# Performance work log

Measured on AMD Instinct MI355X. Metric: run time of the kernel, lower is better.

## Reference

```python
import jax, jax.numpy as jnp
import numpy as np

THR = 1.0   # snntorch default threshold
BETA = 0.9  # beta_val from init_kwargs (clamped to [0,1] in snntorch)
ALPHA_SG = 2.0  # snntorch ATan surrogate default alpha

T, B, IN, H1, H2, OUT = 50, 256, 1536, 4096, 4096, 64


@jax.custom_vjp
def spike_fn(mem_shift):
    # Heaviside spike with ATan surrogate gradient (snntorch default)
    return (mem_shift > 0).astype(mem_shift.dtype)

def _spike_fwd(m):
    return spike_fn(m), m

def _spike_bwd(m, g):
    grad = (ALPHA_SG / 2.0) / (1.0 + (jnp.pi / 2.0 * ALPHA_SG * m) ** 2)
    return (g * grad,)

spike_fn.defvjp(_spike_fwd, _spike_bwd)


def setup_inputs() -> dict:
    key = jax.random.key(0)
    ks = jax.random.split(key, 7)
    spike_seq = (jax.random.uniform(ks[0], (T, B, IN)) < 0.3).astype(jnp.float32)
    def lin(k, fan_out, fan_in):
        bound = 1.0 / np.sqrt(fan_in)
        kw, kb = jax.random.split(k)
        W = jax.random.uniform(kw, (fan_out, fan_in), minval=-bound, maxval=bound, dtype=jnp.float32)
        b = jax.random.uniform(kb, (fan_out,), minval=-bound, maxval=bound, dtype=jnp.float32)
        return W, b
    W1, b1 = lin(ks[1], H1, IN)
    W2, b2 = lin(ks[2], H2, H1)
    W3, b3 = lin(ks[3], OUT, H2)
    return {"spike_seq": spike_seq, "W1": W1, "b1": b1, "W2": W2, "b2": b2, "W3": W3, "b3": b3}


def _lif_step(mem, cur):
    # snntorch Leaky, reset_mechanism='subtract': reset is computed from the
    # PREVIOUS membrane and detached; then mem = beta*mem + cur - reset*thr.
    reset = jax.lax.stop_gradient((mem > THR).astype(cur.dtype))
    mem = BETA * mem + cur - reset * THR
    spk = spike_fn(mem - THR)
    return spk, mem


def reference(spike_seq, W1, b1, W2, b2, W3, b3):
    batch = spike_seq.shape[1]
    dt = spike_seq.dtype
    m1 = jnp.zeros((batch, W1.shape[0]), dt)
    m2 = jnp.zeros((batch, W2.shape[0]), dt)
    m3 = jnp.zeros((batch, W3.shape[0]), dt)
    acc = jnp.zeros((batch, W3.shape[0]), dt)

    def step(carry, x_t):
        m1, m2, m3, acc = carry
        s1, m1 = _lif_step(m1, x_t @ W1.T + b1)
        s2, m2 = _lif_step(m2, s1 @ W2.T + b2)
        s3, m3 = _lif_step(m3, s2 @ W3.T + b3)
        return (m1, m2, m3, acc + s3), None

    (m1, m2, m3, acc), _ = jax.lax.scan(step, (m1, m2, m3, acc), spike_seq)
    return acc
```

## Files before the change

kernel.cpp:

```cpp
#include <hip/hip_runtime.h>
#include <stdint.h>
#include <stddef.h>
#include <math.h>


#define T_STEPS 50
#define BATCH   256
#define N_H     4096
#define DEN     8355711

typedef unsigned short u16;
typedef __attribute__((ext_vector_type(4))) int i32x4;
typedef __attribute__((ext_vector_type(4))) float f32x4;

#define GLL16(gp, lp) __builtin_amdgcn_global_load_lds( \
    (const __attribute__((address_space(1))) void*)(gp), \
    (__attribute__((address_space(3))) void*)(lp), 16, 0, 0)

__global__ __launch_bounds__(256) void zero_ws(float4* __restrict__ p) {
    p[(size_t)blockIdx.x * 256 + threadIdx.x] = make_float4(0.f, 0.f, 0.f, 0.f);
}

__device__ inline void digits3(float w, float inv_s, int& h, int& m, int& l) {
    int V = (int)rintf(w * inv_s);
    V = min(max(V, -DEN), DEN);
    l = ((V + 128) & 255) - 128;
    const int V2 = (V - l) >> 8;
    m = ((V2 + 128) & 255) - 128;
    h = (V2 - m) >> 8;
}

__global__ __launch_bounds__(256)
void split3_i8(const float4* __restrict__ W, char* __restrict__ P,
               size_t plane_elems, float inv_s)
{
    const size_t i = (size_t)blockIdx.x * 256 + threadIdx.x;
    const float4 w = W[i];
    int h0,m0,l0,h1,m1,l1,h2,m2,l2,h3,m3,l3;
    digits3(w.x, inv_s, h0, m0, l0);
    digits3(w.y, inv_s, h1, m1, l1);
    digits3(w.z, inv_s, h2, m2, l2);
    digits3(w.w, inv_s, h3, m3, l3);
    const uint32_t ph = (uint32_t)(uint8_t)h0 | ((uint32_t)(uint8_t)h1 << 8) |
                        ((uint32_t)(uint8_t)h2 << 16) | ((uint32_t)(uint8_t)h3 << 24);
    const uint32_t pm = (uint32_t)(uint8_t)m0 | ((uint32_t)(uint8_t)m1 << 8) |
                        ((uint32_t)(uint8_t)m2 << 16) | ((uint32_t)(uint8_t)m3 << 24);
    const uint32_t pl = (uint32_t)(uint8_t)l0 | ((uint32_t)(uint8_t)l1 << 8) |
                        ((uint32_t)(uint8_t)l2 << 16) | ((uint32_t)(uint8_t)l3 << 24);
    *(uint32_t*)&P[4 * i]                   = ph;
    *(uint32_t*)&P[plane_elems + 4 * i]     = pm;
    *(uint32_t*)&P[2 * plane_elems + 4 * i] = pl;
}

__global__ __launch_bounds__(256)
void xcvt_i8(const float4* __restrict__ in, uint32_t* __restrict__ out) {
    const size_t i = (size_t)blockIdx.x * 256 + threadIdx.x;
    const float4 v = in[i];
    out[i] = (uint32_t)(v.x > 0.5f) | ((uint32_t)(v.y > 0.5f) << 8) |
             ((uint32_t)(v.z > 0.5f) << 16) | ((uint32_t)(v.w > 0.5f) << 24);
}

template<int K>
__global__ __launch_bounds__(256, 2)
void gemm_planes(const char* __restrict__ A, const char* __restrict__ Wp,
                 float* __restrict__ cur, float s_base)
{
    const int ITERS = 3 * K / 64;
    __shared__ char As[2 * 8192];
    __shared__ char Bs[2 * 8192];

    const int tid  = threadIdx.x;
    const int wave = tid >> 6, lane = tid & 63;
    const int wm = wave >> 1, wn = wave & 1;

    const int bid   = blockIdx.x;
    const int cbase = (((bid & 7) << 2) + ((bid >> 3) & 3)) * 128;
    const int abase = (bid >> 5) * 128;

    i32x4 acc[4][4];
    f32x4 facc[4][4];
#pragma unroll
    for (int i = 0; i < 4; ++i)
#pragma unroll
        for (int j = 0; j < 4; ++j) { acc[i][j] = (i32x4)(0); facc[i][j] = (f32x4)(0.f); }

    const int soff0 = wave * 2048 + lane * 16;
    const int soff1 = soff0 + 1024;
    const int r0 = soff0 >> 6, r1 = soff1 >> 6;
    const int kb0 = ((((soff0 >> 4) & 3) ^ ((r0 >> 1) & 3)) << 4);
    const int kb1 = ((((soff1 >> 4) & 3) ^ ((r1 >> 1) & 3)) << 4);

    const size_t aoff0 = (size_t)(abase + r0) * K + kb0;
    const size_t aoff1 = (size_t)(abase + r1) * K + kb1;
    const size_t boff0 = (size_t)(cbase + r0) * K + kb0;
    const size_t boff1 = (size_t)(cbase + r1) * K + kb1;

    const int sbase = wave * 2048;

    const int rlo = lane & 15, rhi = lane >> 4;
    const int qr = (rlo >> 1) & 3;
    const int rdA = (wm * 64 + rlo) * 64 + ((rhi ^ qr) << 4);
    const int rdB = (wn * 64 + rlo) * 64 + ((rhi ^ qr) << 4);

    {
        const char* ak = A;
        const char* bk = Wp;
        GLL16(ak + aoff0, As + sbase);
        GLL16(ak + aoff1, As + sbase + 1024);
        GLL16(bk + boff0, Bs + sbase);
        GLL16(bk + boff1, Bs + sbase + 1024);
    }
    __syncthreads();

    for (int it = 0; it < ITERS; ++it) {
        const int buf = (it & 1) * 8192;
        if (it + 1 < ITERS) {
            const int fn = (it + 1) * 64;
            const int pn = fn / K;
            const int kn = fn - pn * K;
            const int nbuf = 8192 - buf;
            const char* ak = A + kn;
            const char* bk = Wp + (size_t)pn * ((size_t)N_H * K) + kn;
            GLL16(ak + aoff0, As + nbuf + sbase);
            GLL16(ak + aoff1, As + nbuf + sbase + 1024);
            GLL16(bk + boff0, Bs + nbuf + sbase);
            GLL16(bk + boff1, Bs + nbuf + sbase + 1024);
        }

        const char* pAf = As + buf + rdA;
        const char* pBf = Bs + buf + rdB;
        i32x4 av[4], bv[4];
#pragma unroll
        for (int i = 0; i < 4; ++i) av[i] = *(const i32x4*)(pAf + i * 1024);
#pragma unroll
        for (int j = 0; j < 4; ++j) bv[j] = *(const i32x4*)(pBf + j * 1024);
#pragma unroll
        for (int i = 0; i < 4; ++i)
#pragma unroll
            for (int j = 0; j < 4; ++j)
                acc[i][j] = __builtin_amdgcn_mfma_i32_16x16x64_i8(
                    av[i], bv[j], acc[i][j], 0, 0, 0);

        if ((((it + 1) * 64) % K) == 0) {
            const int p = (it * 64) / K;
            const float sc = s_base * (float)(65536 >> (8 * p));
#pragma unroll
            for (int i = 0; i < 4; ++i)
#pragma unroll
                for (int j = 0; j < 4; ++j) {
#pragma unroll
                    for (int r = 0; r < 4; ++r)
                        facc[i][j][r] += sc * (float)acc[i][j][r];
                    acc[i][j] = (i32x4)(0);
                }
        }
        __syncthreads();
    }

    const int orow = abase + wm * 64 + rhi * 4;
    const int ocol = cbase + wn * 64 + rlo;
#pragma unroll
    for (int i = 0; i < 4; ++i)
#pragma unroll
        for (int j = 0; j < 4; ++j)
#pragma unroll
            for (int r = 0; r < 4; ++r)
                cur[(size_t)(orow + i * 16 + r) * N_H + ocol + j * 16] = facc[i][j][r];
}

__global__ __launch_bounds__(256, 2)
void gemm3_i8(const char* __restrict__ A, const char* __restrict__ W3p,
              float* __restrict__ part3, float s_base)
{
    __shared__ char As[2 * 8192];
    __shared__ char Bs[2 * 4096];

    const int tid  = threadIdx.x;
    const int wave = tid >> 6, lane = tid & 63;
    const int wm = wave >> 1, wn = wave & 1;

    const int rowbase = blockIdx.x * 128;
    const int z = blockIdx.y;
    const int p = z >> 1;
    const int kstart = (z & 1) * 2048;

    i32x4 acc[4][2];
#pragma unroll
    for (int i = 0; i < 4; ++i)
#pragma unroll
        for (int j = 0; j < 2; ++j) acc[i][j] = (i32x4)(0);

    const int soff0 = wave * 2048 + lane * 16;
    const int soff1 = soff0 + 1024;
    const int r0 = soff0 >> 6, r1 = soff1 >> 6;
    const int kb0 = ((((soff0 >> 4) & 3) ^ ((r0 >> 1) & 3)) << 4);
    const int kb1 = ((((soff1 >> 4) & 3) ^ ((r1 >> 1) & 3)) << 4);
    const int soffB = tid * 16;
    const int rB = soffB >> 6;
    const int kbB = ((((soffB >> 4) & 3) ^ ((rB >> 1) & 3)) << 4);

    const size_t aoff0 = (size_t)(rowbase + r0) * 4096 + kb0;
    const size_t aoff1 = (size_t)(rowbase + r1) * 4096 + kb1;
    const size_t boff  = (size_t)rB * 4096 + kbB;

    const char* Bp = W3p + (size_t)p * 64 * 4096;
    const int sbase = wave * 2048;
    const int sbaseB = wave * 1024;

    const int rlo = lane & 15, rhi = lane >> 4;
    const int qr = (rlo >> 1) & 3;
    const int rdA = (wm * 64 + rlo) * 64 + ((rhi ^ qr) << 4);
    const int rdB = (wn * 32 + rlo) * 64 + ((rhi ^ qr) << 4);

    {
        GLL16(A + kstart + aoff0, As + sbase);
        GLL16(A + kstart + aoff1, As + sbase + 1024);
        GLL16(Bp + kstart + boff, Bs + sbaseB);
    }
    __syncthreads();

    for (int it = 0; it < 32; ++it) {
        const int bufA = (it & 1) * 8192;
        const int bufB = (it & 1) * 4096;
        if (it + 1 < 32) {
            const int kn = kstart + (it + 1) * 64;
            GLL16(A + kn + aoff0, As + (8192 - bufA) + sbase);
            GLL16(A + kn + aoff1, As + (8192 - bufA) + sbase + 1024);
            GLL16(Bp + kn + boff, Bs + (4096 - bufB) + sbaseB);
        }

        const char* pAf = As + bufA + rdA;
        const char* pBf = Bs + bufB + rdB;
        i32x4 av[4], bv[2];
#pragma unroll
        for (int i = 0; i < 4; ++i) av[i] = *(const i32x4*)(pAf + i * 1024);
#pragma unroll
        for (int j = 0; j < 2; ++j) bv[j] = *(const i32x4*)(pBf + j * 1024);
#pragma unroll
        for (int i = 0; i < 4; ++i)
#pragma unroll
            for (int j = 0; j < 2; ++j)
                acc[i][j] = __builtin_amdgcn_mfma_i32_16x16x64_i8(
                    av[i], bv[j], acc[i][j], 0, 0, 0);
        __syncthreads();
    }

    const float sc = s_base * (float)(65536 >> (8 * p));
    float* pout = part3 + (size_t)z * (12800 * 64);
    const int orow = rowbase + wm * 64 + rhi * 4;
    const int ocol = wn * 32 + rlo;
#pragma unroll
    for (int i = 0; i < 4; ++i)
#pragma unroll
        for (int j = 0; j < 2; ++j)
#pragma unroll
            for (int r = 0; r < 4; ++r)
                pout[(size_t)(orow + i * 16 + r) * 64 + ocol + j * 16] =
                    (float)acc[i][j][r] * sc;
}

__global__ __launch_bounds__(256)
void lif_scan(const float* __restrict__ cur, const float* __restrict__ bias,
              float* __restrict__ mem, char* __restrict__ sout)
{
    const int i4  = blockIdx.x * 256 + threadIdx.x;
    const int col = (i4 << 2) & (N_H - 1);
    const int b   = i4 >> 10;
    const float4 bv = *(const float4*)&bias[col];
    const size_t mbase = (size_t)b * N_H + col;
    float4 m = *(const float4*)&mem[mbase];

    for (int t = 0; t < 25; ++t) {
        const size_t off = ((size_t)t * BATCH + b) * N_H + col;
        const float4 cv = *(const float4*)&cur[off];
        float4 mn;
        { const float c = cv.x + bv.x;
          mn.x = 0.9f * m.x + c - ((m.x > 1.0f) ? 1.0f : 0.0f); }
        { const float c = cv.y + bv.y;
          mn.y = 0.9f * m.y + c - ((m.y > 1.0f) ? 1.0f : 0.0f); }
        { const float c = cv.z + bv.z;
          mn.z = 0.9f * m.z + c - ((m.z > 1.0f) ? 1.0f : 0.0f); }
        { const float c = cv.w + bv.w;
          mn.w = 0.9f * m.w + c - ((m.w > 1.0f) ? 1.0f : 0.0f); }
        const uint32_t sp = (uint32_t)(mn.x > 1.0f) | ((uint32_t)(mn.y > 1.0f) << 8) |
                            ((uint32_t)(mn.z > 1.0f) << 16) | ((uint32_t)(mn.w > 1.0f) << 24);
        *(uint32_t*)&sout[off] = sp;
        m = mn;
    }
    *(float4*)&mem[mbase] = m;
}

template<int NG>
__global__ __launch_bounds__(256)
void lif3_scan(const float* __restrict__ part, const float* __restrict__ b3,
               float* __restrict__ out)
{
    const int g = blockIdx.x * 256 + threadIdx.x;
    const int j = g & 63;
    const int b = g >> 6;
    const float bj = b3[j];
    float m = 0.f, accum = 0.f;
    for (int t = 0; t < T_STEPS; ++t) {
        const size_t row = (size_t)t * 256 + b;
        float cur = bj;
#pragma unroll
        for (int q = 0; q < NG; ++q)
            cur += part[(size_t)q * (12800 * 64) + row * 64 + j];
        const float reset = (m > 1.0f) ? 1.0f : 0.0f;
        m = 0.9f * m + cur - reset;
        accum += (m > 1.0f) ? 1.0f : 0.0f;
    }
    out[g] = accum;
}

template<int K, bool PACK_BITS>
__global__ __launch_bounds__(512)
void gemm_lif(const float* __restrict__ A, const float* __restrict__ W,
              const float* __restrict__ bias, float* __restrict__ mem,
              float* __restrict__ s_f32, uint32_t* __restrict__ s_bits)
{
    __shared__ float Asf[32][68];
    __shared__ float Wsf[32][68];
    __shared__ uint8_t us[64][64];

    const int tid = threadIdx.x;
    const int abase = blockIdx.y * 64;
    const int cbase = blockIdx.x * 64;
    const int tx = tid & 15;
    const int ty = tid >> 4;

    float acc[2][4];
#pragma unroll
    for (int i = 0; i < 2; ++i)
#pragma unroll
        for (int j = 0; j < 4; ++j) acc[i][j] = 0.f;

    const int lrow = tid >> 3;
    const int lg = tid & 7;

    for (int k0 = 0; k0 < K; k0 += 32) {
        const float4 av = *(const float4*)&A[(size_t)(abase + lrow) * K + k0 + lg * 4];
        const float4 wv = *(const float4*)&W[(size_t)(cbase + lrow) * K + k0 + lg * 4];
        __syncthreads();
        Asf[lg * 4 + 0][lrow] = av.x; Asf[lg * 4 + 1][lrow] = av.y;
        Asf[lg * 4 + 2][lrow] = av.z; Asf[lg * 4 + 3][lrow] = av.w;
        Wsf[lg * 4 + 0][lrow] = wv.x; Wsf[lg * 4 + 1][lrow] = wv.y;
        Wsf[lg * 4 + 2][lrow] = wv.z; Wsf[lg * 4 + 3][lrow] = wv.w;
        __syncthreads();
#pragma unroll
        for (int kk = 0; kk < 32; ++kk) {
            const float2 a2 = *(const float2*)&Asf[kk][ty * 2];
            const float4 b4 = *(const float4*)&Wsf[kk][tx * 4];
            acc[0][0] += a2.x * b4.x; acc[0][1] += a2.x * b4.y;
            acc[0][2] += a2.x * b4.z; acc[0][3] += a2.x * b4.w;
            acc[1][0] += a2.y * b4.x; acc[1][1] += a2.y * b4.y;
            acc[1][2] += a2.y * b4.z; acc[1][3] += a2.y * b4.w;
        }
    }

    const int r0 = abase + ty * 2;
    const int c0loc = tx * 4;
    const int c0 = cbase + c0loc;
    const float4 bv = *(const float4*)&bias[c0];

#pragma unroll
    for (int i = 0; i < 2; ++i) {
        const size_t off = (size_t)(r0 + i) * N_H + c0;
        const float4 mp = *(const float4*)&mem[off];
        float4 mn, sp;
        { float cur = acc[i][0] + bv.x;
          mn.x = 0.9f * mp.x + cur - ((mp.x > 1.0f) ? 1.0f : 0.0f);
          sp.x = (mn.x > 1.0f) ? 1.0f : 0.0f; }
        { float cur = acc[i][1] + bv.y;
          mn.y = 0.9f * mp.y + cur - ((mp.y > 1.0f) ? 1.0f : 0.0f);
          sp.y = (mn.y > 1.0f) ? 1.0f : 0.0f; }
        { float cur = acc[i][2] + bv.z;
          mn.z = 0.9f * mp.z + cur - ((mp.z > 1.0f) ? 1.0f : 0.0f);
          sp.z = (mn.z > 1.0f) ? 1.0f : 0.0f; }
        { float cur = acc[i][3] + bv.w;
          mn.w = 0.9f * mp.w + cur - ((mp.w > 1.0f) ? 1.0f : 0.0f);
          sp.w = (mn.w > 1.0f) ? 1.0f : 0.0f; }
        *(float4*)&mem[off] = mn;
        if constexpr (!PACK_BITS) {
            *(float4*)&s_f32[off] = sp;
        } else {
            us[ty * 2 + i][c0loc + 0] = (uint8_t)sp.x;
            us[ty * 2 + i][c0loc + 1] = (uint8_t)sp.y;
            us[ty * 2 + i][c0loc + 2] = (uint8_t)sp.z;
            us[ty * 2 + i][c0loc + 3] = (uint8_t)sp.w;
        }
    }

    if constexpr (PACK_BITS) {
        __syncthreads();
        if (tid < 128) {
            const int r = tid >> 1;
            const int w = tid & 1;
            uint32_t bits = 0;
#pragma unroll
            for (int b = 0; b < 32; ++b)
                bits |= ((uint32_t)us[r][w * 32 + b]) << b;
            s_bits[(size_t)(abase + r) * 128 + (cbase >> 5) + w] = bits;
        }
    }
}

__global__ __launch_bounds__(256)
void gemm3_bits(const uint32_t* __restrict__ s_bits, const float* __restrict__ W3,
                float* __restrict__ part)
{
    __shared__ float Asf[32][68];
    __shared__ float Wsf[32][68];

    const int tid = threadIdx.x;
    const int rowbase = blockIdx.x * 64;
    const int ks = blockIdx.y;
    const int tx = tid & 15;
    const int ty = tid >> 4;

    float acc[4][4];
#pragma unroll
    for (int i = 0; i < 4; ++i)
#pragma unroll
        for (int j = 0; j < 4; ++j) acc[i][j] = 0.f;

    const int r  = tid & 63;
    const int q  = tid >> 6;
    const int wr = tid >> 3;
    const int wg = tid & 7;

    for (int c = 0; c < 32; ++c) {
        const int k0 = ks * 1024 + c * 32;
        const uint32_t word = s_bits[(size_t)(rowbase + r) * 128 + (k0 >> 5)];
        const float4 wv0 = *(const float4*)&W3[(size_t)wr * 4096 + k0 + wg * 4];
        const float4 wv1 = *(const float4*)&W3[(size_t)(wr + 32) * 4096 + k0 + wg * 4];
        __syncthreads();
#pragma unroll
        for (int u = 0; u < 8; ++u)
            Asf[q * 8 + u][r] = (float)((word >> (q * 8 + u)) & 1u);
        Wsf[wg * 4 + 0][wr] = wv0.x;
        Wsf[wg * 4 + 1][wr] = wv0.y;
        Wsf[wg * 4 + 2][wr] = wv0.z;
        Wsf[wg * 4 + 3][wr] = wv0.w;
        Wsf[wg * 4 + 0][wr + 32] = wv1.x;
        Wsf[wg * 4 + 1][wr + 32] = wv1.y;
        Wsf[wg * 4 + 2][wr + 32] = wv1.z;
        Wsf[wg * 4 + 3][wr + 32] = wv1.w;
        __syncthreads();
#pragma unroll
        for (int kk = 0; kk < 32; ++kk) {
            const float4 a4 = *(const float4*)&Asf[kk][ty * 4];
            const float4 b4 = *(const float4*)&Wsf[kk][tx * 4];
            acc[0][0] += a4.x * b4.x; acc[0][1] += a4.x * b4.y;
            acc[0][2] += a4.x * b4.z; acc[0][3] += a4.x * b4.w;
            acc[1][0] += a4.y * b4.x; acc[1][1] += a4.y * b4.y;
            acc[1][2] += a4.y * b4.z; acc[1][3] += a4.y * b4.w;
            acc[2][0] += a4.z * b4.x; acc[2][1] += a4.z * b4.y;
            acc[2][2] += a4.z * b4.z; acc[2][3] += a4.z * b4.w;
            acc[3][0] += a4.w * b4.x; acc[3][1] += a4.w * b4.y;
            acc[3][2] += a4.w * b4.z; acc[3][3] += a4.w * b4.w;
        }
    }
#pragma unroll
    for (int i = 0; i < 4; ++i) {
        float4 v = make_float4(acc[i][0], acc[i][1], acc[i][2], acc[i][3]);
        *(float4*)&part[((size_t)ks * 12800 + rowbase + ty * 4 + i) * 64 + tx * 4] = v;
    }
}

extern "C" void kernel_launch(void* const* d_in, const int* in_sizes, int n_in,
                              void* d_out, int out_size, void* d_ws, size_t ws_size,
                              hipStream_t stream)
{
    const float* x  = (const float*)d_in[0];
    const float* W1 = (const float*)d_in[1];
    const float* b1 = (const float*)d_in[2];
    const float* W2 = (const float*)d_in[3];
    const float* b2 = (const float*)d_in[4];
    const float* W3 = (const float*)d_in[5];
    const float* b3 = (const float*)d_in[6];

    char* ws = (char*)d_ws;

    const size_t oW1p = 0;
    const size_t oW2p = 18874368;
    const size_t oW3p = 69206016;
    const size_t oXi8 = 69992448;
    const size_t oS1  = 89653248;
    const size_t oS2  = 115867648;
    const size_t oM1  = 168296448;
    const size_t oM2  = 172490752;
    const size_t oCur = 176685056;
    const size_t NEED = 281542656;

    const double bnd1 = 1.0 / sqrt(1536.0);
    const double bnd2 = 1.0 / 64.0;
    const double bnd3 = 1.0 / 64.0;
    const float inv1 = (float)((double)DEN / bnd1), sb1 = (float)(bnd1 / (double)DEN);
    const float inv2 = (float)((double)DEN / bnd2), sb2 = (float)(bnd2 / (double)DEN);
    const float inv3 = (float)((double)DEN / bnd3), sb3 = (float)(bnd3 / (double)DEN);

    if (ws_size >= NEED) {
        char*  W1p  = ws + oW1p;
        char*  W2p  = ws + oW2p;
        char*  W3p  = ws + oW3p;
        char*  xi8  = ws + oXi8;
        char*  s1   = ws + oS1;
        char*  s2   = ws + oS2;
        float* m1   = (float*)(ws + oM1);
        float* m2   = (float*)(ws + oM2);
        float* cur  = (float*)(ws + oCur);
        float* part3 = cur;

        split3_i8<<<6144, 256, 0, stream>>>((const float4*)W1, W1p,
                                            (size_t)4096 * 1536, inv1);
        split3_i8<<<16384, 256, 0, stream>>>((const float4*)W2, W2p,
                                             (size_t)4096 * 4096, inv2);
        split3_i8<<<256, 256, 0, stream>>>((const float4*)W3, W3p,
                                           (size_t)64 * 4096, inv3);
        xcvt_i8<<<19200, 256, 0, stream>>>((const float4*)x, (uint32_t*)xi8);
        zero_ws<<<2048, 256, 0, stream>>>((float4*)m1);

        const size_t chunk_rows = (size_t)25 * BATCH;
        for (int chunk = 0; chunk < 2; ++chunk) {
            gemm_planes<1536><<<1600, 256, 0, stream>>>(
                xi8 + chunk * chunk_rows * 1536, W1p, cur, sb1);
            lif_scan<<<1024, 256, 0, stream>>>(cur, b1, m1, s1);
            gemm_planes<4096><<<1600, 256, 0, stream>>>(s1, W2p, cur, sb2);
            lif_scan<<<1024, 256, 0, stream>>>(cur, b2, m2,
                                               s2 + chunk * chunk_rows * N_H);
        }
        gemm3_i8<<<dim3(100, 6), 256, 0, stream>>>(s2, W3p, part3, sb3);
        lif3_scan<6><<<64, 256, 0, stream>>>(part3, b3, (float*)d_out);
    } else {
        float*    m1     = (float*)(ws);
        float*    m2     = (float*)(ws + (size_t)4 * 1024 * 1024);
        float*    s1f    = (float*)(ws + (size_t)8 * 1024 * 1024);
        uint32_t* s2bits = (uint32_t*)(ws + (size_t)12 * 1024 * 1024);
        float*    part   = (float*)(ws + (size_t)20 * 1024 * 1024);

        zero_ws<<<2048, 256, 0, stream>>>((float4*)m1);
        for (int t = 0; t < T_STEPS; ++t) {
            gemm_lif<1536, false><<<dim3(64, 4), 512, 0, stream>>>(
                x + (size_t)t * BATCH * 1536, W1, b1, m1, s1f, nullptr);
            gemm_lif<4096, true><<<dim3(64, 4), 512, 0, stream>>>(
                s1f, W2, b2, m2, nullptr, s2bits + (size_t)t * BATCH * 128);
        }
        gemm3_bits<<<dim3(200, 4), 256, 0, stream>>>(s2bits, W3, part);
        lif3_scan<4><<<64, 256, 0, stream>>>(part, b3, (float*)d_out);
    }
}
```

Measured before the change: 1.519 ms.

## Add 4-slot LDS ring pipeline GEMM with 256x128 tiles and register prefetch

```diff
diff --git a/kernel.cpp b/kernel.cpp
--- a/kernel.cpp
+++ b/kernel.cpp
@@ -61,6 +61,127 @@
 }
 
 template<int K>
+__global__ __launch_bounds__(512, 2)
+void gemm_planes_ring(const char* __restrict__ A, const char* __restrict__ Wp,
+                      float* __restrict__ cur, float s_base)
+{
+    const int ITERS = 3 * K / 64;
+    const int SLOT  = 24576;
+    extern __shared__ char Lds[];
+
+    const int tid  = threadIdx.x;
+    const int wave = tid >> 6, lane = tid & 63;
+    const int wr = wave >> 1, wc = wave & 1;
+
+    const int bid   = blockIdx.x;
+    const int cbase = (((bid & 7) << 2) + ((bid >> 3) & 3)) * 128;
+    const int abase = (bid >> 5) * 256;
+
+    i32x4 acc[4][4];
+    f32x4 facc[4][4];
+#pragma unroll
+    for (int i = 0; i < 4; ++i)
+#pragma unroll
+        for (int j = 0; j < 4; ++j) { acc[i][j] = (i32x4)(0); facc[i][j] = (f32x4)(0.f); }
+
+    const int soff = tid * 16;
+    const int rs   = soff >> 6;
+    const int cs   = (soff >> 4) & 3;
+    const int kbs  = ((cs ^ ((rs >> 1) & 3)) << 4);
+    const size_t aoff0 = (size_t)(abase + rs) * K + kbs;
+    const size_t aoff1 = aoff0 + (size_t)128 * K;
+    const size_t boff  = (size_t)(cbase + rs) * K + kbs;
+    const int dstA0 = wave * 1024;
+    const int dstA1 = 8192 + wave * 1024;
+    const int dstB  = 16384 + wave * 1024;
+
+    const int rlo = lane & 15, rhi = lane >> 4;
+    const int qr  = (rlo >> 1) & 3;
+    const int rdA = (wr * 64 + rlo) * 64 + ((rhi ^ qr) << 4);
+    const int rdB = 16384 + (wc * 64 + rlo) * 64 + ((rhi ^ qr) << 4);
+
+    auto stage = [&](int u) {
+        const int pn = (u * 64) / K;
+        const int kn = u * 64 - pn * K;
+        char* slot = Lds + (u & 3) * SLOT;
+        const char* ak = A + kn;
+        const char* bk = Wp + (size_t)pn * ((size_t)N_H * K) + kn;
+        GLL16(ak + aoff0, slot + dstA0);
+        GLL16(ak + aoff1, slot + dstA1);
+        GLL16(bk + boff,  slot + dstB);
+    };
+
+    stage(0); stage(1); stage(2);
+    asm volatile("s_waitcnt vmcnt(6)" ::: "memory");
+    __builtin_amdgcn_s_barrier();
+    asm volatile("" ::: "memory");
+
+    i32x4 avA[4], bvA[4], avB[4], bvB[4];
+    {
+        const char* nb = Lds;
+#pragma unroll
+        for (int i = 0; i < 4; ++i) avA[i] = *(const i32x4*)(nb + rdA + i * 1024);
+#pragma unroll
+        for (int j = 0; j < 4; ++j) bvA[j] = *(const i32x4*)(nb + rdB + j * 1024);
+    }
+
+#define RING_BODY(tt, avC, bvC, avN, bvN)                                     \
+    {                                                                         \
+        if ((tt) + 2 < ITERS) { asm volatile("s_waitcnt vmcnt(3)" ::: "memory"); } \
+        else                  { asm volatile("s_waitcnt vmcnt(0)" ::: "memory"); } \
+        __builtin_amdgcn_s_barrier();                                         \
+        asm volatile("" ::: "memory");                                        \
+        if ((tt) + 3 < ITERS) stage((tt) + 3);                                \
+        if ((tt) + 1 < ITERS) {                                               \
+            const char* nb_ = Lds + (((tt) + 1) & 3) * SLOT;                  \
+            _Pragma("unroll")                                                 \
+            for (int i = 0; i < 4; ++i)                                       \
+                avN[i] = *(const i32x4*)(nb_ + rdA + i * 1024);               \
+            _Pragma("unroll")                                                 \
+            for (int j = 0; j < 4; ++j)                                       \
+                bvN[j] = *(const i32x4*)(nb_ + rdB + j * 1024);               \
+        }                                                                     \
+        __builtin_amdgcn_s_setprio(1);                                        \
+        _Pragma("unroll")                                                     \
+        for (int i = 0; i < 4; ++i)                                           \
+            _Pragma("unroll")                                                 \
+            for (int j = 0; j < 4; ++j)                                       \
+                acc[i][j] = __builtin_amdgcn_mfma_i32_16x16x64_i8(            \
+                    avC[i], bvC[j], acc[i][j], 0, 0, 0);                      \
+        __builtin_amdgcn_s_setprio(0);                                        \
+        if (((((tt) + 1) * 64) % K) == 0) {                                   \
+            const int p_ = ((tt) * 64) / K;                                   \
+            const float sc_ = s_base * (float)(65536 >> (8 * p_));            \
+            _Pragma("unroll")                                                 \
+            for (int i = 0; i < 4; ++i)                                       \
+                _Pragma("unroll")                                             \
+                for (int j = 0; j < 4; ++j) {                                 \
+                    _Pragma("unroll")                                         \
+                    for (int r = 0; r < 4; ++r)                               \
+                        facc[i][j][r] += sc_ * (float)acc[i][j][r];           \
+                    acc[i][j] = (i32x4)(0);                                   \
+                }                                                             \
+        }                                                                     \
+    }
+
+    for (int t = 0; t < ITERS; t += 2) {
+        RING_BODY(t,     avA, bvA, avB, bvB);
+        RING_BODY(t + 1, avB, bvB, avA, bvA);
+    }
+#undef RING_BODY
+
+    const int orow = abase + wr * 64 + rhi * 4;
+    const int ocol = cbase + wc * 64 + rlo;
+#pragma unroll
+    for (int i = 0; i < 4; ++i)
+#pragma unroll
+        for (int j = 0; j < 4; ++j)
+#pragma unroll
+            for (int r = 0; r < 4; ++r)
+                cur[(size_t)(orow + i * 16 + r) * N_H + ocol + j * 16] = facc[i][j][r];
+}
+
+template<int K>
 __global__ __launch_bounds__(256, 2)
 void gemm_planes(const char* __restrict__ A, const char* __restrict__ Wp,
                  float* __restrict__ cur, float s_base)
@@ -103,12 +224,10 @@
     const int rdB = (wn * 64 + rlo) * 64 + ((rhi ^ qr) << 4);
 
     {
-        const char* ak = A;
-        const char* bk = Wp;
-        GLL16(ak + aoff0, As + sbase);
-        GLL16(ak + aoff1, As + sbase + 1024);
-        GLL16(bk + boff0, Bs + sbase);
-        GLL16(bk + boff1, Bs + sbase + 1024);
+        GLL16(A + aoff0, As + sbase);
+        GLL16(A + aoff1, As + sbase + 1024);
+        GLL16(Wp + boff0, Bs + sbase);
+        GLL16(Wp + boff1, Bs + sbase + 1024);
     }
     __syncthreads();
 
@@ -500,6 +619,16 @@
     const float inv2 = (float)((double)DEN / bnd2), sb2 = (float)(bnd2 / (double)DEN);
     const float inv3 = (float)((double)DEN / bnd3), sb3 = (float)(bnd3 / (double)DEN);
 
+    static const bool ring_ok = []() {
+        hipError_t e1 = hipFuncSetAttribute(
+            reinterpret_cast<const void*>(&gemm_planes_ring<1536>),
+            hipFuncAttributeMaxDynamicSharedMemorySize, 98304);
+        hipError_t e2 = hipFuncSetAttribute(
+            reinterpret_cast<const void*>(&gemm_planes_ring<4096>),
+            hipFuncAttributeMaxDynamicSharedMemorySize, 98304);
+        return e1 == hipSuccess && e2 == hipSuccess;
+    }();
+
     if (ws_size >= NEED) {
         char*  W1p  = ws + oW1p;
         char*  W2p  = ws + oW2p;
@@ -523,10 +652,20 @@
 
         const size_t chunk_rows = (size_t)25 * BATCH;
         for (int chunk = 0; chunk < 2; ++chunk) {
-            gemm_planes<1536><<<1600, 256, 0, stream>>>(
-                xi8 + chunk * chunk_rows * 1536, W1p, cur, sb1);
+            if (ring_ok) {
+                gemm_planes_ring<1536><<<800, 512, 98304, stream>>>(
+                    xi8 + chunk * chunk_rows * 1536, W1p, cur, sb1);
+            } else {
+                gemm_planes<1536><<<1600, 256, 0, stream>>>(
+                    xi8 + chunk * chunk_rows * 1536, W1p, cur, sb1);
+            }
             lif_scan<<<1024, 256, 0, stream>>>(cur, b1, m1, s1);
-            gemm_planes<4096><<<1600, 256, 0, stream>>>(s1, W2p, cur, sb2);
+            if (ring_ok) {
+                gemm_planes_ring<4096><<<800, 512, 98304, stream>>>(
+                    s1, W2p, cur, sb2);
+            } else {
+                gemm_planes<4096><<<1600, 256, 0, stream>>>(s1, W2p, cur, sb2);
+            }
             lif_scan<<<1024, 256, 0, stream>>>(cur, b2, m2,
                                                s2 + chunk * chunk_rows * N_H);
         }
```

Result: faster. 1.389 ms (-8.5%).

## Restructure int8 plane GEMM with 4-slot A pipeline and direct B register loads

Applied to the files above, without the earlier changes.

```diff
diff --git a/kernel.cpp b/kernel.cpp
--- a/kernel.cpp
+++ b/kernel.cpp
@@ -61,21 +61,20 @@
 }
 
 template<int K>
-__global__ __launch_bounds__(256, 2)
-void gemm_planes(const char* __restrict__ A, const char* __restrict__ Wp,
-                 float* __restrict__ cur, float s_base)
+__global__ __launch_bounds__(512, 2)
+void gemm_planes_bd(const char* __restrict__ A, const char* __restrict__ Wp,
+                    float* __restrict__ cur, float s_base)
 {
     const int ITERS = 3 * K / 64;
-    __shared__ char As[2 * 8192];
-    __shared__ char Bs[2 * 8192];
+    __shared__ char As[4][16384];
 
     const int tid  = threadIdx.x;
     const int wave = tid >> 6, lane = tid & 63;
-    const int wm = wave >> 1, wn = wave & 1;
+    const int wr = wave >> 1, wc = wave & 1;
 
     const int bid   = blockIdx.x;
     const int cbase = (((bid & 7) << 2) + ((bid >> 3) & 3)) * 128;
-    const int abase = (bid >> 5) * 128;
+    const int abase = (bid >> 5) * 256;
 
     i32x4 acc[4][4];
     f32x4 facc[4][4];
@@ -84,81 +83,103 @@
 #pragma unroll
         for (int j = 0; j < 4; ++j) { acc[i][j] = (i32x4)(0); facc[i][j] = (f32x4)(0.f); }
 
-    const int soff0 = wave * 2048 + lane * 16;
-    const int soff1 = soff0 + 1024;
-    const int r0 = soff0 >> 6, r1 = soff1 >> 6;
-    const int kb0 = ((((soff0 >> 4) & 3) ^ ((r0 >> 1) & 3)) << 4);
-    const int kb1 = ((((soff1 >> 4) & 3) ^ ((r1 >> 1) & 3)) << 4);
-
-    const size_t aoff0 = (size_t)(abase + r0) * K + kb0;
-    const size_t aoff1 = (size_t)(abase + r1) * K + kb1;
-    const size_t boff0 = (size_t)(cbase + r0) * K + kb0;
-    const size_t boff1 = (size_t)(cbase + r1) * K + kb1;
-
-    const int sbase = wave * 2048;
+    const int soff = tid * 16;
+    const int rs   = soff >> 6;
+    const int cs   = (soff >> 4) & 3;
+    const int kbs  = ((cs ^ ((rs >> 1) & 3)) << 4);
+    const size_t aoff0 = (size_t)(abase + rs) * K + kbs;
+    const size_t aoff1 = aoff0 + (size_t)128 * K;
+    const int dstA0 = wave * 1024;
+    const int dstA1 = 8192 + wave * 1024;
 
     const int rlo = lane & 15, rhi = lane >> 4;
-    const int qr = (rlo >> 1) & 3;
-    const int rdA = (wm * 64 + rlo) * 64 + ((rhi ^ qr) << 4);
-    const int rdB = (wn * 64 + rlo) * 64 + ((rhi ^ qr) << 4);
+    const int qr  = (rlo >> 1) & 3;
+    const int rdA = (wr * 64 + rlo) * 64 + ((rhi ^ qr) << 4);
+
+    const size_t bb0 = (size_t)(cbase + wc * 64 +  0 + rlo) * K + rhi * 16;
+    const size_t bb1 = (size_t)(cbase + wc * 64 + 16 + rlo) * K + rhi * 16;
+    const size_t bb2 = (size_t)(cbase + wc * 64 + 32 + rlo) * K + rhi * 16;
+    const size_t bb3 = (size_t)(cbase + wc * 64 + 48 + rlo) * K + rhi * 16;
+
+    auto stage = [&](int u, char* slot) {
+        const int pn = (u * 64) / K;
+        const int kn = u * 64 - pn * K;
+        const char* ak = A + kn;
+        GLL16(ak + aoff0, slot + dstA0);
+        GLL16(ak + aoff1, slot + dstA1);
+    };
+
+    i32x4 avA[4], bvA[4], avB[4], bvB[4];
 
     {
-        const char* ak = A;
         const char* bk = Wp;
-        GLL16(ak + aoff0, As + sbase);
-        GLL16(ak + aoff1, As + sbase + 1024);
-        GLL16(bk + boff0, Bs + sbase);
-        GLL16(bk + boff1, Bs + sbase + 1024);
-    }
-    __syncthreads();
-
-    for (int it = 0; it < ITERS; ++it) {
-        const int buf = (it & 1) * 8192;
-        if (it + 1 < ITERS) {
-            const int fn = (it + 1) * 64;
-            const int pn = fn / K;
-            const int kn = fn - pn * K;
-            const int nbuf = 8192 - buf;
-            const char* ak = A + kn;
-            const char* bk = Wp + (size_t)pn * ((size_t)N_H * K) + kn;
-            GLL16(ak + aoff0, As + nbuf + sbase);
-            GLL16(ak + aoff1, As + nbuf + sbase + 1024);
-            GLL16(bk + boff0, Bs + nbuf + sbase);
-            GLL16(bk + boff1, Bs + nbuf + sbase + 1024);
-        }
-
-        const char* pAf = As + buf + rdA;
-        const char* pBf = Bs + buf + rdB;
-        i32x4 av[4], bv[4];
-#pragma unroll
-        for (int i = 0; i < 4; ++i) av[i] = *(const i32x4*)(pAf + i * 1024);
-#pragma unroll
-        for (int j = 0; j < 4; ++j) bv[j] = *(const i32x4*)(pBf + j * 1024);
-#pragma unroll
-        for (int i = 0; i < 4; ++i)
-#pragma unroll
-            for (int j = 0; j < 4; ++j)
-                acc[i][j] = __builtin_amdgcn_mfma_i32_16x16x64_i8(
-                    av[i], bv[j], acc[i][j], 0, 0, 0);
-
-        if ((((it + 1) * 64) % K) == 0) {
-            const int p = (it * 64) / K;
-            const float sc = s_base * (float)(65536 >> (8 * p));
-#pragma unroll
-            for (int i = 0; i < 4; ++i)
-#pragma unroll
-                for (int j = 0; j < 4; ++j) {
-#pragma unroll
-                    for (int r = 0; r < 4; ++r)
-                        facc[i][j][r] += sc * (float)acc[i][j][r];
-                    acc[i][j] = (i32x4)(0);
-                }
-        }
-        __syncthreads();
-    }
-
-    const int orow = abase + wm * 64 + rhi * 4;
-    const int ocol = cbase + wn * 64 + rlo;
+        bvA[0] = *(const i32x4*)(bk + bb0);
+        bvA[1] = *(const i32x4*)(bk + bb1);
+        bvA[2] = *(const i32x4*)(bk + bb2);
+        bvA[3] = *(const i32x4*)(bk + bb3);
+    }
+    stage(0, &As[0][0]); stage(1, &As[1][0]); stage(2, &As[2][0]);
+    asm volatile("s_waitcnt vmcnt(4)" ::: "memory");
+    __builtin_amdgcn_s_barrier();
+    asm volatile("" ::: "memory");
+#pragma unroll
+    for (int i = 0; i < 4; ++i) avA[i] = *(const i32x4*)(&As[0][0] + rdA + i * 1024);
+
+#define BD_BODY(tt, NSLOT, SSLOT, avC, bvC, avN, bvN)                         \
+    {                                                                         \
+        if ((tt) + 2 < ITERS) { asm volatile("s_waitcnt vmcnt(2)" ::: "memory"); } \
+        else                  { asm volatile("s_waitcnt vmcnt(0)" ::: "memory"); } \
+        __builtin_amdgcn_s_barrier();                                         \
+        asm volatile("" ::: "memory");                                        \
+        if ((tt) + 1 < ITERS) {                                               \
+            const int pn_ = (((tt) + 1) * 64) / K;                            \
+            const int kn_ = ((tt) + 1) * 64 - pn_ * K;                        \
+            const char* bk_ = Wp + (size_t)pn_ * ((size_t)N_H * K) + kn_;     \
+            bvN[0] = *(const i32x4*)(bk_ + bb0);                              \
+            bvN[1] = *(const i32x4*)(bk_ + bb1);                              \
+            bvN[2] = *(const i32x4*)(bk_ + bb2);                              \
+            bvN[3] = *(const i32x4*)(bk_ + bb3);                              \
+        }                                                                     \
+        if ((tt) + 3 < ITERS) stage((tt) + 3, &As[SSLOT][0]);                 \
+        if ((tt) + 1 < ITERS) {                                               \
+            const char* nb_ = &As[NSLOT][0];                                  \
+            _Pragma("unroll")                                                 \
+            for (int i = 0; i < 4; ++i)                                       \
+                avN[i] = *(const i32x4*)(nb_ + rdA + i * 1024);               \
+        }                                                                     \
+        __builtin_amdgcn_s_setprio(1);                                        \
+        _Pragma("unroll")                                                     \
+        for (int i = 0; i < 4; ++i)                                           \
+            _Pragma("unroll")                                                 \
+            for (int j = 0; j < 4; ++j)                                       \
+                acc[i][j] = __builtin_amdgcn_mfma_i32_16x16x64_i8(            \
+                    avC[i], bvC[j], acc[i][j], 0, 0, 0);                      \
+        __builtin_amdgcn_s_setprio(0);                                        \
+        if (((((tt) + 1) * 64) % K) == 0) {                                   \
+            const int p_ = ((tt) * 64) / K;                                   \
+            const float sc_ = s_base * (float)(65536 >> (8 * p_));            \
+            _Pragma("unroll")                                                 \
+            for (int i = 0; i < 4; ++i)                                       \
+                _Pragma("unroll")                                             \
+                for (int j = 0; j < 4; ++j) {                                 \
+                    _Pragma("unroll")                                         \
+                    for (int r = 0; r < 4; ++r)                               \
+                        facc[i][j][r] += sc_ * (float)acc[i][j][r];           \
+                    acc[i][j] = (i32x4)(0);                                   \
+                }                                                             \
+        }                                                                     \
+    }
+
+    for (int t = 0; t < ITERS; t += 4) {
+        BD_BODY(t + 0, 1, 3, avA, bvA, avB, bvB);
+        BD_BODY(t + 1, 2, 0, avB, bvB, avA, bvA);
+        BD_BODY(t + 2, 3, 1, avA, bvA, avB, bvB);
+        BD_BODY(t + 3, 0, 2, avB, bvB, avA, bvA);
+    }
+#undef BD_BODY
+
+    const int orow = abase + wr * 64 + rhi * 4;
+    const int ocol = cbase + wc * 64 + rlo;
 #pragma unroll
     for (int i = 0; i < 4; ++i)
 #pragma unroll
@@ -523,10 +544,10 @@
 
         const size_t chunk_rows = (size_t)25 * BATCH;
         for (int chunk = 0; chunk < 2; ++chunk) {
-            gemm_planes<1536><<<1600, 256, 0, stream>>>(
+            gemm_planes_bd<1536><<<800, 512, 0, stream>>>(
                 xi8 + chunk * chunk_rows * 1536, W1p, cur, sb1);
             lif_scan<<<1024, 256, 0, stream>>>(cur, b1, m1, s1);
-            gemm_planes<4096><<<1600, 256, 0, stream>>>(s1, W2p, cur, sb2);
+            gemm_planes_bd<4096><<<800, 512, 0, stream>>>(s1, W2p, cur, sb2);
             lif_scan<<<1024, 256, 0, stream>>>(cur, b2, m2,
                                                s2 + chunk * chunk_rows * N_H);
         }
```

Result: slower. 2.948 ms (+94.2%).
